# Kernel tuning notes

Hardware: AMD Instinct MI355X
Metric: run time of the kernel (lower is better)

Reference implementation:

```python
import jax, jax.numpy as jnp
import numpy as np

B, N, DIM = 32, 1024, 768
H, S, D = 16, 4, 64  # num_heads, num_subheads (L=H*S=64), attn_dim


def setup_inputs() -> dict:
    key = jax.random.key(0)
    k1, k2, k3, k4 = jax.random.split(key, 4)
    x = jax.random.normal(k1, (B, N, DIM), dtype=jnp.float32)
    eos_indices = jax.random.randint(k2, (B,), 0, N)
    # q_emb: original shape (1,H,S,1,D); singleton dims dropped -> (H,S,D)
    q_emb = jax.random.normal(k3, (H, S, D), dtype=jnp.float32)
    # k Linear(dim -> H*D), xavier-uniform weight, zero bias (share_kv: v == k)
    limit = float(np.sqrt(6.0 / (DIM + H * D)))
    Wk = jax.random.uniform(k4, (DIM, H * D), dtype=jnp.float32, minval=-limit, maxval=limit)
    bk = jnp.zeros((H * D,), dtype=jnp.float32)
    return {"x": x, "eos_indices": eos_indices, "q_emb": q_emb, "Wk": Wk, "bk": bk}


def reference(x, eos_indices, q_emb, Wk, bk):
    # x: (B,N,dim); shared k/v projection -> (B,N,H,D)
    kv = (x @ Wk + bk).reshape(x.shape[0], x.shape[1], H, D)
    scale = D ** -0.5
    # Avoid the torch expand over subheads: contract directly.
    # logits: (B,H,S,N)
    logits = jnp.einsum("hsd,bnhd->bhsn", q_emb * scale, kv)
    # eos masking: positions strictly after eos index are masked out
    mask = jnp.arange(x.shape[1])[None, None, None, :] > eos_indices[:, None, None, None]
    logits = jnp.where(mask, -jnp.inf, logits)
    attn = jax.nn.softmax(logits, axis=-1)
    # weighted sum over N -> (B,H,S,D) -> (B,L,D)
    out = jnp.einsum("bhsn,bnhd->bhsd", attn, kv)
    return out.reshape(x.shape[0], H * S, D)
```

## Files before the change

kernel.cpp:

```cpp
#include <hip/hip_runtime.h>
#include <hip/hip_bf16.h>
#include <stdint.h>

typedef float  f32x4  __attribute__((ext_vector_type(4)));
typedef __bf16 bf16x4 __attribute__((ext_vector_type(4)));
typedef __bf16 bf16x8 __attribute__((ext_vector_type(8)));
typedef unsigned int u32x2 __attribute__((ext_vector_type(2)));
typedef unsigned int u32x4 __attribute__((ext_vector_type(4)));

#define AS1 __attribute__((address_space(1)))
#define AS3 __attribute__((address_space(3)))

__device__ __forceinline__ void async_load16(const void* g, void* lds) {
    __builtin_amdgcn_global_load_lds((const AS1 unsigned int*)g,
                                     (AS3 unsigned int*)lds, 16, 0, 0);
}

__global__ __launch_bounds__(256) void qw_kernel(const float* __restrict__ q_emb,
                                                 const float* __restrict__ wk,
                                                 __bf16* __restrict__ qwT) {
    __shared__ float qlds[256];
    __shared__ float part[4096];
    const int t = threadIdx.x;
    const int kc = blockIdx.x;
    const int h  = blockIdx.y;
    const int k0 = kc * 64;
    qlds[t] = q_emb[h * 256 + t] * 0.125f;
    __syncthreads();
    const int dseg = t & 15;
    const int krow = t >> 4;
#pragma unroll
    for (int i = 0; i < 4; ++i) {
        const int k = i * 16 + krow;
        f32x4 wv = *(const f32x4*)&wk[(size_t)(k0 + k) * 1024 + h * 64 + dseg * 4];
#pragma unroll
        for (int s = 0; s < 4; ++s) {
            float p = qlds[s * 64 + dseg * 4 + 0] * wv[0]
                    + qlds[s * 64 + dseg * 4 + 1] * wv[1]
                    + qlds[s * 64 + dseg * 4 + 2] * wv[2]
                    + qlds[s * 64 + dseg * 4 + 3] * wv[3];
            part[k * 64 + s * 16 + dseg] = p;
        }
    }
    __syncthreads();
    const int k = t >> 2, s = t & 3;
    const float* pp = &part[k * 64 + s * 16];
    float sum = 0.f;
#pragma unroll
    for (int j = 0; j < 16; ++j) sum += pp[j];
    qwT[(h * 4 + s) * 768 + k0 + k] = (__bf16)sum;
}

__global__ __launch_bounds__(512) void logits_kernel(const float* __restrict__ x,
                                                     const __bf16* __restrict__ qwT,
                                                     const int* __restrict__ eos_idx,
                                                     float* __restrict__ Lg,
                                                     float* __restrict__ partials) {
    __shared__ char smem[49152];
    char* Bl = smem;
    char* Al = smem + 16384;
    const int t = threadIdx.x, l = t & 63, w = t >> 6;
    const int m0 = blockIdx.x * 128;
    const int bb = m0 >> 10, n0 = m0 & 1023;
    const int chunk = blockIdx.x & 7;
    const int wrA = (w >> 1) * 32;
    const int wcB = (w & 1) * 32;

    f32x4 acc[2][2];
#pragma unroll
    for (int i = 0; i < 2; ++i)
#pragma unroll
        for (int j = 0; j < 2; ++j) acc[i][j] = (f32x4)0.f;

    const int Bcol = t >> 3, Bseg = t & 7;
    const __bf16* qsrc = qwT + Bcol * 768 + (Bseg ^ (Bcol & 7)) * 8;
    const int Arow0 = t >> 4;
    const int Aseg = t & 15;

    f32x4 av[4];
    async_load16(qsrc, Bl + t * 16);
#pragma unroll
    for (int i = 0; i < 4; ++i)
        av[i] = *(const f32x4*)&x[(size_t)(m0 + i * 32 + Arow0) * 768 + Aseg * 4];
#pragma unroll
    for (int i = 0; i < 4; ++i) {
        const int row = i * 32 + Arow0;
        bf16x4 vv = {(__bf16)av[i][0], (__bf16)av[i][1], (__bf16)av[i][2], (__bf16)av[i][3]};
        *(bf16x4*)(Al + ((row * 128 + Aseg * 8) ^ ((row & 7) << 4))) = vv;
    }
    asm volatile("s_waitcnt vmcnt(0)" ::: "memory");
    __syncthreads();

    int buf = 0;
    for (int step = 0; step < 12; ++step) {
        const int nbuf = buf ^ 1;
        const bool more = (step + 1) < 12;
        if (more) {
            const int kt = (step + 1) * 64;
            async_load16(qsrc + kt, Bl + nbuf * 8192 + t * 16);
#pragma unroll
            for (int i = 0; i < 4; ++i)
                av[i] = *(const f32x4*)&x[(size_t)(m0 + i * 32 + Arow0) * 768 + kt + Aseg * 4];
        }
#pragma unroll
        for (int kh = 0; kh < 2; ++kh) {
            const int u = kh * 4 + (l >> 4);
            bf16x8 af[2], bfr[2];
#pragma unroll
            for (int i = 0; i < 2; ++i) {
                const int row = wrA + i * 16 + (l & 15);
                af[i] = *(const bf16x8*)(Al + buf * 16384 +
                                         ((row * 128 + u * 16) ^ ((row & 7) << 4)));
            }
#pragma unroll
            for (int j = 0; j < 2; ++j) {
                const int col = wcB + j * 16 + (l & 15);
                bfr[j] = *(const bf16x8*)(Bl + buf * 8192 +
                                          ((col * 128 + u * 16) ^ ((col & 7) << 4)));
            }
#pragma unroll
            for (int i = 0; i < 2; ++i)
#pragma unroll
                for (int j = 0; j < 2; ++j)
                    acc[i][j] = __builtin_amdgcn_mfma_f32_16x16x32_bf16(
                        af[i], bfr[j], acc[i][j], 0, 0, 0);
        }
        if (more) {
#pragma unroll
            for (int i = 0; i < 4; ++i) {
                const int row = i * 32 + Arow0;
                bf16x4 vv = {(__bf16)av[i][0], (__bf16)av[i][1], (__bf16)av[i][2], (__bf16)av[i][3]};
                *(bf16x4*)(Al + nbuf * 16384 + ((row * 128 + Aseg * 8) ^ ((row & 7) << 4))) = vv;
            }
        }
        asm volatile("s_waitcnt vmcnt(0)" ::: "memory");
        __syncthreads();
        buf = nbuf;
    }

#pragma unroll
    for (int i = 0; i < 2; ++i)
#pragma unroll
        for (int j = 0; j < 2; ++j) {
            const int hs = wcB + j * 16 + (l & 15);
            const int nb = wrA + i * 16 + (l >> 4) * 4;
            *(f32x4*)(smem + ((hs * 512 + nb * 4) ^ ((hs & 7) << 4))) = acc[i][j];
        }
    __syncthreads();
    const int eosb = eos_idx[bb];
    const int hs = t >> 3;
    f32x4 vv[4];
    float mx = -INFINITY;
#pragma unroll
    for (int i = 0; i < 4; ++i) {
        const int seg = (t & 7) + i * 8;
        f32x4 v = *(const f32x4*)(smem + ((hs * 512 + seg * 16) ^ ((hs & 7) << 4)));
#pragma unroll
        for (int j = 0; j < 4; ++j) {
            if (n0 + seg * 4 + j > eosb) v[j] = -INFINITY;
            mx = fmaxf(mx, v[j]);
        }
        vv[i] = v;
        *(f32x4*)&Lg[(size_t)bb * 65536 + hs * 1024 + n0 + seg * 4] = v;
    }
#pragma unroll
    for (int off = 1; off < 8; off <<= 1) mx = fmaxf(mx, __shfl_xor(mx, off));
    float sl = 0.f;
    if (mx > -INFINITY) {
#pragma unroll
        for (int i = 0; i < 4; ++i)
#pragma unroll
            for (int j = 0; j < 4; ++j) sl += __expf(vv[i][j] - mx);
    }
#pragma unroll
    for (int off = 1; off < 8; off <<= 1) sl += __shfl_xor(sl, off);
    if ((t & 7) == 0) {
        float2 st = {mx, sl};
        *(float2*)&partials[(size_t)(((bb * 8 + chunk) * 64) + hs) * 2] = st;
    }
}

__global__ __launch_bounds__(256) void pv_kernel(const float* __restrict__ x,
                                                 const float* __restrict__ Lg,
                                                 const float* __restrict__ partials,
                                                 float* __restrict__ y) {
    __shared__ char smem[32768];
    char* Pl = smem;
    char* Xl = smem + 16384;
    const int t = threadIdx.x, l = t & 63, w = t >> 6;
    const int vid = (blockIdx.x & 7) * 48 + (blockIdx.x >> 3);
    const int b = vid / 12, kc = vid % 12;
    const int k0 = kc * 64;
    const int wrA = (w >> 1) * 32, wcB = (w & 1) * 32;
    const float* Lgb = Lg + (size_t)b * 65536;
    const float* xb = x + (size_t)b * 786432 + k0 + l;
    const int fK = ((l & 7) << 4) | (((l >> 3) & 1) << 3);

    const int r0 = t >> 3, r1 = 32 + (t >> 3);
    float m0r, i0r, m1r, i1r;
    {
        const float* pb = partials + (size_t)b * 1024;
        float m = -INFINITY, m2 = -INFINITY;
#pragma unroll
        for (int c = 0; c < 8; ++c) {
            m  = fmaxf(m,  pb[(c * 64 + r0) * 2]);
            m2 = fmaxf(m2, pb[(c * 64 + r1) * 2]);
        }
        float s = 0.f, s2 = 0.f;
#pragma unroll
        for (int c = 0; c < 8; ++c) {
            float2 p0 = *(const float2*)&pb[(c * 64 + r0) * 2];
            float2 p1 = *(const float2*)&pb[(c * 64 + r1) * 2];
            s  += p0.y * __expf(p0.x - m);
            s2 += p1.y * __expf(p1.x - m2);
        }
        m0r = m; i0r = 1.0f / s;
        m1r = m2; i1r = 1.0f / s2;
    }
    const int n0s0 = (((t & 7) ^ (r0 & 7)) * 8);
    const int n0s1 = (((t & 7) ^ (r1 & 7)) * 8);

    f32x4 acc[2][2];
#pragma unroll
    for (int i = 0; i < 2; ++i)
#pragma unroll
        for (int j = 0; j < 2; ++j) acc[i][j] = (f32x4)0.f;

    float xv[16];
#pragma unroll
    for (int ii = 0; ii < 2; ++ii) {
        const int r = ii ? r1 : r0;
        const int ns = ii ? n0s1 : n0s0;
        const float mr = ii ? m1r : m0r, ir = ii ? i1r : i0r;
        f32x4 lo = *(const f32x4*)&Lgb[(size_t)r * 1024 + ns];
        f32x4 hi = *(const f32x4*)&Lgb[(size_t)r * 1024 + ns + 4];
        bf16x8 pk;
#pragma unroll
        for (int j = 0; j < 4; ++j) pk[j]     = (__bf16)(__expf(lo[j] - mr) * ir);
#pragma unroll
        for (int j = 0; j < 4; ++j) pk[4 + j] = (__bf16)(__expf(hi[j] - mr) * ir);
        *(bf16x8*)(Pl + ii * 4096 + t * 16) = pk;
    }
#pragma unroll
    for (int i = 0; i < 4; ++i)
#pragma unroll
        for (int j = 0; j < 4; ++j)
            xv[i * 4 + j] = xb[(size_t)(i * 16 + w * 4 + j) * 768];
#pragma unroll
    for (int i = 0; i < 4; ++i) {
        bf16x4 vv = {(__bf16)xv[i * 4 + 0], (__bf16)xv[i * 4 + 1],
                     (__bf16)xv[i * 4 + 2], (__bf16)xv[i * 4 + 3]};
        const int nb2 = (i * 16 + w * 4) * 2;
        *(bf16x4*)(Xl + ((l * 128 + nb2) ^ fK)) = vv;
    }
    __syncthreads();

    int buf = 0;
    for (int step = 0; step < 16; ++step) {
        const int nbuf = buf ^ 1;
        const bool more = (step + 1) < 16;
        if (more) {
            const int nt = (step + 1) * 64;
#pragma unroll
            for (int ii = 0; ii < 2; ++ii) {
                const int r = ii ? r1 : r0;
                const int ns = ii ? n0s1 : n0s0;
                const float mr = ii ? m1r : m0r, ir = ii ? i1r : i0r;
                f32x4 lo = *(const f32x4*)&Lgb[(size_t)r * 1024 + nt + ns];
                f32x4 hi = *(const f32x4*)&Lgb[(size_t)r * 1024 + nt + ns + 4];
                bf16x8 pk;
#pragma unroll
                for (int j = 0; j < 4; ++j) pk[j]     = (__bf16)(__expf(lo[j] - mr) * ir);
#pragma unroll
                for (int j = 0; j < 4; ++j) pk[4 + j] = (__bf16)(__expf(hi[j] - mr) * ir);
                *(bf16x8*)(Pl + nbuf * 8192 + ii * 4096 + t * 16) = pk;
            }
#pragma unroll
            for (int i = 0; i < 4; ++i)
#pragma unroll
                for (int j = 0; j < 4; ++j)
                    xv[i * 4 + j] = xb[(size_t)(nt + i * 16 + w * 4 + j) * 768];
        }
#pragma unroll
        for (int kh = 0; kh < 2; ++kh) {
            const int u = kh * 4 + (l >> 4);
            bf16x8 af[2], bfr[2];
#pragma unroll
            for (int i = 0; i < 2; ++i) {
                const int row = wrA + i * 16 + (l & 15);
                af[i] = *(const bf16x8*)(Pl + buf * 8192 +
                                         ((row * 128 + u * 16) ^ ((row & 7) << 4)));
            }
#pragma unroll
            for (int j = 0; j < 2; ++j) {
                const int kcol = wcB + j * 16 + (l & 15);
                const int fKc = ((kcol & 7) << 4) | (((kcol >> 3) & 1) << 3);
                const int addrA = kcol * 128 + kh * 64 + (l >> 4) * 16;
                u32x2 lo = *(const u32x2*)(Xl + buf * 8192 + (addrA ^ fKc));
                u32x2 hi = *(const u32x2*)(Xl + buf * 8192 + ((addrA + 8) ^ fKc));
                u32x4 uu = {lo[0], lo[1], hi[0], hi[1]};
                bfr[j] = __builtin_bit_cast(bf16x8, uu);
            }
#pragma unroll
            for (int i = 0; i < 2; ++i)
#pragma unroll
                for (int j = 0; j < 2; ++j)
                    acc[i][j] = __builtin_amdgcn_mfma_f32_16x16x32_bf16(
                        af[i], bfr[j], acc[i][j], 0, 0, 0);
        }
        if (more) {
#pragma unroll
            for (int i = 0; i < 4; ++i) {
                bf16x4 vv = {(__bf16)xv[i * 4 + 0], (__bf16)xv[i * 4 + 1],
                             (__bf16)xv[i * 4 + 2], (__bf16)xv[i * 4 + 3]};
                const int nb2 = (i * 16 + w * 4) * 2;
                *(bf16x4*)(Xl + nbuf * 8192 + ((l * 128 + nb2) ^ fK)) = vv;
            }
        }
        __syncthreads();
        buf = nbuf;
    }

#pragma unroll
    for (int i = 0; i < 2; ++i)
#pragma unroll
        for (int j = 0; j < 2; ++j) {
            const int kcol = wcB + j * 16 + (l & 15);
#pragma unroll
            for (int r = 0; r < 4; ++r) {
                const int hs2 = wrA + i * 16 + (l >> 4) * 4 + r;
                *(float*)(smem + ((hs2 * 256 + kcol * 4) ^ ((hs2 & 7) << 4))) = acc[i][j][r];
            }
        }
    __syncthreads();
    const int hs2 = t >> 2;
#pragma unroll
    for (int i = 0; i < 4; ++i) {
        const int seg = (t & 3) + i * 4;
        f32x4 v = *(const f32x4*)(smem + ((hs2 * 256 + seg * 16) ^ ((hs2 & 7) << 4)));
        *(f32x4*)&y[(size_t)(b * 64 + hs2) * 768 + k0 + seg * 4] = v;
    }
}

__global__ __launch_bounds__(256) void out_kernel(const float* __restrict__ y,
                                                  const float* __restrict__ wk,
                                                  const float* __restrict__ bk,
                                                  float* __restrict__ out) {
    __shared__ float ylds[8 * 768];
    __shared__ float red[2048];
    const int t = threadIdx.x;
    const int vid = (blockIdx.x & 7) * 32 + (blockIdx.x >> 3);
    const int h = vid >> 4, bp = vid & 15;
#pragma unroll
    for (int r = 0; r < 8; ++r) {
        const int gb = bp * 2 + (r >> 2);
        const int hs = h * 4 + (r & 3);
#pragma unroll
        for (int i = 0; i < 3; ++i)
            ylds[r * 768 + i * 256 + t] = y[(size_t)(gb * 64 + hs) * 768 + i * 256 + t];
    }
    __syncthreads();
    const int kp = t >> 6, d = t & 63;
    float acc[8] = {0.f, 0.f, 0.f, 0.f, 0.f, 0.f, 0.f, 0.f};
    for (int i = 0; i < 48; ++i) {
        const int k = kp * 192 + i * 4;
        const float wv0 = wk[(size_t)(k + 0) * 1024 + h * 64 + d];
        const float wv1 = wk[(size_t)(k + 1) * 1024 + h * 64 + d];
        const float wv2 = wk[(size_t)(k + 2) * 1024 + h * 64 + d];
        const float wv3 = wk[(size_t)(k + 3) * 1024 + h * 64 + d];
#pragma unroll
        for (int r = 0; r < 8; ++r) {
            f32x4 yv = *(const f32x4*)&ylds[r * 768 + k];
            acc[r] += yv[0] * wv0 + yv[1] * wv1 + yv[2] * wv2 + yv[3] * wv3;
        }
    }
#pragma unroll
    for (int r = 0; r < 8; ++r) red[(r * 64 + d) * 4 + kp] = acc[r];
    __syncthreads();
#pragma unroll
    for (int i = 0; i < 2; ++i) {
        const int o = i * 256 + t;
        const int r = o >> 6, dd = o & 63;
        f32x4 pv = *(const f32x4*)&red[o * 4];
        const float s = pv[0] + pv[1] + pv[2] + pv[3] + bk[h * 64 + dd];
        const int gb = bp * 2 + (r >> 2);
        out[(size_t)(gb * 64 + h * 4 + (r & 3)) * 64 + dd] = s;
    }
}

extern "C" void kernel_launch(void* const* d_in, const int* in_sizes, int n_in,
                              void* d_out, int out_size, void* d_ws, size_t ws_size,
                              hipStream_t stream) {
    const float* x     = (const float*)d_in[0];
    const int*   eos   = (const int*)d_in[1];
    const float* q_emb = (const float*)d_in[2];
    const float* Wk    = (const float*)d_in[3];
    const float* bk    = (const float*)d_in[4];
    float* out = (float*)d_out;

    char* ws = (char*)d_ws;
    __bf16* qwT      = (__bf16*)ws;
    float*  Lg       = (float*)(ws + 131072);
    float*  partials = (float*)(ws + 131072 + 8388608);
    float*  y        = (float*)(ws + 131072 + 8388608 + 131072);

    qw_kernel<<<dim3(12, 16), 256, 0, stream>>>(q_emb, Wk, qwT);
    logits_kernel<<<dim3(256), 512, 0, stream>>>(x, qwT, eos, Lg, partials);
    pv_kernel<<<dim3(384), 256, 0, stream>>>(x, Lg, partials, y);
    out_kernel<<<dim3(256), 256, 0, stream>>>(y, Wk, bk, out);
}
```

Baseline: 63.83 us.

## Halve tile sizes in logits and PV kernels to double grid parallelism

The logits kernel now processes 64 rows per block instead of 128, doubling the grid to 512 blocks and using 16 softmax partial chunks per batch. The PV kernel splits the sequence dimension into two halves, doubling its grid to 768 blocks and writing two partial y buffers, which the out kernel sums when loading. Launch bounds are tightened so more blocks fit per CU. The intent is to fill the 256 CUs better on this memory-bound pipeline, at the cost of extra partial-sum traffic, an extra y buffer read, and less reuse per block.

```diff
diff --git a/kernel.cpp b/kernel.cpp
--- a/kernel.cpp
+++ b/kernel.cpp
@@ -51,42 +51,41 @@
     qwT[(h * 4 + s) * 768 + k0 + k] = (__bf16)sum;
 }
 
-__global__ __launch_bounds__(512) void logits_kernel(const float* __restrict__ x,
-                                                     const __bf16* __restrict__ qwT,
-                                                     const int* __restrict__ eos_idx,
-                                                     float* __restrict__ Lg,
-                                                     float* __restrict__ partials) {
-    __shared__ char smem[49152];
+__global__ __launch_bounds__(512, 4) void logits_kernel(const float* __restrict__ x,
+                                                        const __bf16* __restrict__ qwT,
+                                                        const int* __restrict__ eos_idx,
+                                                        float* __restrict__ Lg,
+                                                        float* __restrict__ partials) {
+    __shared__ char smem[32768];
     char* Bl = smem;
     char* Al = smem + 16384;
     const int t = threadIdx.x, l = t & 63, w = t >> 6;
-    const int m0 = blockIdx.x * 128;
+    const int m0 = blockIdx.x * 64;
     const int bb = m0 >> 10, n0 = m0 & 1023;
-    const int chunk = blockIdx.x & 7;
-    const int wrA = (w >> 1) * 32;
-    const int wcB = (w & 1) * 32;
-
-    f32x4 acc[2][2];
-#pragma unroll
-    for (int i = 0; i < 2; ++i)
-#pragma unroll
-        for (int j = 0; j < 2; ++j) acc[i][j] = (f32x4)0.f;
+    const int chunk = (m0 >> 6) & 15;
+    const int wm = (w >> 1) * 16;
+    const int wh = (w & 1) * 32;
+
+    f32x4 acc[2];
+    acc[0] = (f32x4)0.f; acc[1] = (f32x4)0.f;
 
     const int Bcol = t >> 3, Bseg = t & 7;
     const __bf16* qsrc = qwT + Bcol * 768 + (Bseg ^ (Bcol & 7)) * 8;
-    const int Arow0 = t >> 4;
-    const int Aseg = t & 15;
-
-    f32x4 av[4];
+    const int Arow = t >> 3;
+    const float* xrow = &x[(size_t)(m0 + Arow) * 768 + (t & 7) * 8];
+    const int Adst = (Arow * 128 + (t & 7) * 16) ^ ((Arow & 7) << 4);
+
+    f32x4 av0, av1;
     async_load16(qsrc, Bl + t * 16);
-#pragma unroll
-    for (int i = 0; i < 4; ++i)
-        av[i] = *(const f32x4*)&x[(size_t)(m0 + i * 32 + Arow0) * 768 + Aseg * 4];
-#pragma unroll
-    for (int i = 0; i < 4; ++i) {
-        const int row = i * 32 + Arow0;
-        bf16x4 vv = {(__bf16)av[i][0], (__bf16)av[i][1], (__bf16)av[i][2], (__bf16)av[i][3]};
-        *(bf16x4*)(Al + ((row * 128 + Aseg * 8) ^ ((row & 7) << 4))) = vv;
+    av0 = *(const f32x4*)(xrow);
+    av1 = *(const f32x4*)(xrow + 4);
+    {
+        bf16x8 v;
+        v[0] = (__bf16)av0[0]; v[1] = (__bf16)av0[1];
+        v[2] = (__bf16)av0[2]; v[3] = (__bf16)av0[3];
+        v[4] = (__bf16)av1[0]; v[5] = (__bf16)av1[1];
+        v[6] = (__bf16)av1[2]; v[7] = (__bf16)av1[3];
+        *(bf16x8*)(Al + Adst) = v;
     }
     asm volatile("s_waitcnt vmcnt(0)" ::: "memory");
     __syncthreads();
@@ -98,40 +97,33 @@
         if (more) {
             const int kt = (step + 1) * 64;
             async_load16(qsrc + kt, Bl + nbuf * 8192 + t * 16);
-#pragma unroll
-            for (int i = 0; i < 4; ++i)
-                av[i] = *(const f32x4*)&x[(size_t)(m0 + i * 32 + Arow0) * 768 + kt + Aseg * 4];
+            av0 = *(const f32x4*)(xrow + kt);
+            av1 = *(const f32x4*)(xrow + kt + 4);
         }
 #pragma unroll
         for (int kh = 0; kh < 2; ++kh) {
             const int u = kh * 4 + (l >> 4);
-            bf16x8 af[2], bfr[2];
-#pragma unroll
-            for (int i = 0; i < 2; ++i) {
-                const int row = wrA + i * 16 + (l & 15);
-                af[i] = *(const bf16x8*)(Al + buf * 16384 +
-                                         ((row * 128 + u * 16) ^ ((row & 7) << 4)));
-            }
+            const int arow = wm + (l & 15);
+            bf16x8 af = *(const bf16x8*)(Al + buf * 8192 +
+                                         ((arow * 128 + u * 16) ^ ((arow & 7) << 4)));
+            bf16x8 bfr[2];
 #pragma unroll
             for (int j = 0; j < 2; ++j) {
-                const int col = wcB + j * 16 + (l & 15);
+                const int col = wh + j * 16 + (l & 15);
                 bfr[j] = *(const bf16x8*)(Bl + buf * 8192 +
                                           ((col * 128 + u * 16) ^ ((col & 7) << 4)));
             }
 #pragma unroll
-            for (int i = 0; i < 2; ++i)
-#pragma unroll
-                for (int j = 0; j < 2; ++j)
-                    acc[i][j] = __builtin_amdgcn_mfma_f32_16x16x32_bf16(
-                        af[i], bfr[j], acc[i][j], 0, 0, 0);
+            for (int j = 0; j < 2; ++j)
+                acc[j] = __builtin_amdgcn_mfma_f32_16x16x32_bf16(af, bfr[j], acc[j], 0, 0, 0);
         }
         if (more) {
-#pragma unroll
-            for (int i = 0; i < 4; ++i) {
-                const int row = i * 32 + Arow0;
-                bf16x4 vv = {(__bf16)av[i][0], (__bf16)av[i][1], (__bf16)av[i][2], (__bf16)av[i][3]};
-                *(bf16x4*)(Al + nbuf * 16384 + ((row * 128 + Aseg * 8) ^ ((row & 7) << 4))) = vv;
-            }
+            bf16x8 v;
+            v[0] = (__bf16)av0[0]; v[1] = (__bf16)av0[1];
+            v[2] = (__bf16)av0[2]; v[3] = (__bf16)av0[3];
+            v[4] = (__bf16)av1[0]; v[5] = (__bf16)av1[1];
+            v[6] = (__bf16)av1[2]; v[7] = (__bf16)av1[3];
+            *(bf16x8*)(Al + nbuf * 8192 + Adst) = v;
         }
         asm volatile("s_waitcnt vmcnt(0)" ::: "memory");
         __syncthreads();
@@ -139,58 +131,54 @@
     }
 
 #pragma unroll
-    for (int i = 0; i < 2; ++i)
-#pragma unroll
-        for (int j = 0; j < 2; ++j) {
-            const int hs = wcB + j * 16 + (l & 15);
-            const int nb = wrA + i * 16 + (l >> 4) * 4;
-            *(f32x4*)(smem + ((hs * 512 + nb * 4) ^ ((hs & 7) << 4))) = acc[i][j];
-        }
+    for (int j = 0; j < 2; ++j) {
+        const int hs = wh + j * 16 + (l & 15);
+        const int nb = wm + (l >> 4) * 4;
+        *(f32x4*)(smem + ((hs * 256 + nb * 4) ^ ((hs & 7) << 4))) = acc[j];
+    }
     __syncthreads();
     const int eosb = eos_idx[bb];
-    const int hs = t >> 3;
-    f32x4 vv[4];
+    const int hs = t >> 3, seg = t & 7;
+    const int fH = (hs & 7) << 4;
+    f32x4 v0 = *(const f32x4*)(smem + ((hs * 256 + seg * 32) ^ fH));
+    f32x4 v1 = *(const f32x4*)(smem + ((hs * 256 + seg * 32 + 16) ^ fH));
+    const int nbase = n0 + seg * 8;
     float mx = -INFINITY;
 #pragma unroll
-    for (int i = 0; i < 4; ++i) {
-        const int seg = (t & 7) + i * 8;
-        f32x4 v = *(const f32x4*)(smem + ((hs * 512 + seg * 16) ^ ((hs & 7) << 4)));
-#pragma unroll
-        for (int j = 0; j < 4; ++j) {
-            if (n0 + seg * 4 + j > eosb) v[j] = -INFINITY;
-            mx = fmaxf(mx, v[j]);
-        }
-        vv[i] = v;
-        *(f32x4*)&Lg[(size_t)bb * 65536 + hs * 1024 + n0 + seg * 4] = v;
-    }
+    for (int j = 0; j < 4; ++j) {
+        if (nbase + j > eosb) v0[j] = -INFINITY;
+        if (nbase + 4 + j > eosb) v1[j] = -INFINITY;
+        mx = fmaxf(mx, fmaxf(v0[j], v1[j]));
+    }
+    *(f32x4*)&Lg[(size_t)bb * 65536 + hs * 1024 + nbase] = v0;
+    *(f32x4*)&Lg[(size_t)bb * 65536 + hs * 1024 + nbase + 4] = v1;
 #pragma unroll
     for (int off = 1; off < 8; off <<= 1) mx = fmaxf(mx, __shfl_xor(mx, off));
     float sl = 0.f;
     if (mx > -INFINITY) {
 #pragma unroll
-        for (int i = 0; i < 4; ++i)
-#pragma unroll
-            for (int j = 0; j < 4; ++j) sl += __expf(vv[i][j] - mx);
+        for (int j = 0; j < 4; ++j) sl += __expf(v0[j] - mx) + __expf(v1[j] - mx);
     }
 #pragma unroll
     for (int off = 1; off < 8; off <<= 1) sl += __shfl_xor(sl, off);
-    if ((t & 7) == 0) {
+    if (seg == 0) {
         float2 st = {mx, sl};
-        *(float2*)&partials[(size_t)(((bb * 8 + chunk) * 64) + hs) * 2] = st;
-    }
-}
-
-__global__ __launch_bounds__(256) void pv_kernel(const float* __restrict__ x,
-                                                 const float* __restrict__ Lg,
-                                                 const float* __restrict__ partials,
-                                                 float* __restrict__ y) {
+        *(float2*)&partials[(size_t)(((bb * 16 + chunk) * 64) + hs) * 2] = st;
+    }
+}
+
+__global__ __launch_bounds__(256, 3) void pv_kernel(const float* __restrict__ x,
+                                                    const float* __restrict__ Lg,
+                                                    const float* __restrict__ partials,
+                                                    float* __restrict__ y) {
     __shared__ char smem[32768];
     char* Pl = smem;
     char* Xl = smem + 16384;
     const int t = threadIdx.x, l = t & 63, w = t >> 6;
-    const int vid = (blockIdx.x & 7) * 48 + (blockIdx.x >> 3);
-    const int b = vid / 12, kc = vid % 12;
-    const int k0 = kc * 64;
+    const int vid = (blockIdx.x & 7) * 96 + (blockIdx.x >> 3);
+    const int b = vid / 24, rem = vid % 24;
+    const int kc = rem % 12, nh = rem / 12;
+    const int k0 = kc * 64, nbase = nh * 512;
     const int wrA = (w >> 1) * 32, wcB = (w & 1) * 32;
     const float* Lgb = Lg + (size_t)b * 65536;
     const float* xb = x + (size_t)b * 786432 + k0 + l;
@@ -199,16 +187,16 @@
     const int r0 = t >> 3, r1 = 32 + (t >> 3);
     float m0r, i0r, m1r, i1r;
     {
-        const float* pb = partials + (size_t)b * 1024;
+        const float* pb = partials + (size_t)b * 2048;
         float m = -INFINITY, m2 = -INFINITY;
 #pragma unroll
-        for (int c = 0; c < 8; ++c) {
+        for (int c = 0; c < 16; ++c) {
             m  = fmaxf(m,  pb[(c * 64 + r0) * 2]);
             m2 = fmaxf(m2, pb[(c * 64 + r1) * 2]);
         }
         float s = 0.f, s2 = 0.f;
 #pragma unroll
-        for (int c = 0; c < 8; ++c) {
+        for (int c = 0; c < 16; ++c) {
             float2 p0 = *(const float2*)&pb[(c * 64 + r0) * 2];
             float2 p1 = *(const float2*)&pb[(c * 64 + r1) * 2];
             s  += p0.y * __expf(p0.x - m);
@@ -227,54 +215,48 @@
         for (int j = 0; j < 2; ++j) acc[i][j] = (f32x4)0.f;
 
     float xv[16];
-#pragma unroll
-    for (int ii = 0; ii < 2; ++ii) {
-        const int r = ii ? r1 : r0;
-        const int ns = ii ? n0s1 : n0s0;
-        const float mr = ii ? m1r : m0r, ir = ii ? i1r : i0r;
-        f32x4 lo = *(const f32x4*)&Lgb[(size_t)r * 1024 + ns];
-        f32x4 hi = *(const f32x4*)&Lgb[(size_t)r * 1024 + ns + 4];
+    f32x4 plo0, phi0, plo1, phi1;
+
+    plo0 = *(const f32x4*)&Lgb[(size_t)r0 * 1024 + nbase + n0s0];
+    phi0 = *(const f32x4*)&Lgb[(size_t)r0 * 1024 + nbase + n0s0 + 4];
+    plo1 = *(const f32x4*)&Lgb[(size_t)r1 * 1024 + nbase + n0s1];
+    phi1 = *(const f32x4*)&Lgb[(size_t)r1 * 1024 + nbase + n0s1 + 4];
+#pragma unroll
+    for (int i = 0; i < 4; ++i)
+#pragma unroll
+        for (int j = 0; j < 4; ++j)
+            xv[i * 4 + j] = xb[(size_t)(nbase + i * 16 + w * 4 + j) * 768];
+    {
         bf16x8 pk;
 #pragma unroll
-        for (int j = 0; j < 4; ++j) pk[j]     = (__bf16)(__expf(lo[j] - mr) * ir);
-#pragma unroll
-        for (int j = 0; j < 4; ++j) pk[4 + j] = (__bf16)(__expf(hi[j] - mr) * ir);
-        *(bf16x8*)(Pl + ii * 4096 + t * 16) = pk;
-    }
-#pragma unroll
-    for (int i = 0; i < 4; ++i)
-#pragma unroll
-        for (int j = 0; j < 4; ++j)
-            xv[i * 4 + j] = xb[(size_t)(i * 16 + w * 4 + j) * 768];
-#pragma unroll
-    for (int i = 0; i < 4; ++i) {
-        bf16x4 vv = {(__bf16)xv[i * 4 + 0], (__bf16)xv[i * 4 + 1],
-                     (__bf16)xv[i * 4 + 2], (__bf16)xv[i * 4 + 3]};
-        const int nb2 = (i * 16 + w * 4) * 2;
-        *(bf16x4*)(Xl + ((l * 128 + nb2) ^ fK)) = vv;
+        for (int j = 0; j < 4; ++j) pk[j]     = (__bf16)(__expf(plo0[j] - m0r) * i0r);
+#pragma unroll
+        for (int j = 0; j < 4; ++j) pk[4 + j] = (__bf16)(__expf(phi0[j] - m0r) * i0r);
+        *(bf16x8*)(Pl + t * 16) = pk;
+#pragma unroll
+        for (int j = 0; j < 4; ++j) pk[j]     = (__bf16)(__expf(plo1[j] - m1r) * i1r);
+#pragma unroll
+        for (int j = 0; j < 4; ++j) pk[4 + j] = (__bf16)(__expf(phi1[j] - m1r) * i1r);
+        *(bf16x8*)(Pl + 4096 + t * 16) = pk;
+#pragma unroll
+        for (int i = 0; i < 4; ++i) {
+            bf16x4 vv = {(__bf16)xv[i * 4 + 0], (__bf16)xv[i * 4 + 1],
+                         (__bf16)xv[i * 4 + 2], (__bf16)xv[i * 4 + 3]};
+            *(bf16x4*)(Xl + ((l * 128 + (i * 16 + w * 4) * 2) ^ fK)) = vv;
+        }
     }
     __syncthreads();
 
     int buf = 0;
-    for (int step = 0; step < 16; ++step) {
+    for (int step = 0; step < 8; ++step) {
         const int nbuf = buf ^ 1;
-        const bool more = (step + 1) < 16;
+        const bool more = (step + 1) < 8;
         if (more) {
-            const int nt = (step + 1) * 64;
-#pragma unroll
-            for (int ii = 0; ii < 2; ++ii) {
-                const int r = ii ? r1 : r0;
-                const int ns = ii ? n0s1 : n0s0;
-                const float mr = ii ? m1r : m0r, ir = ii ? i1r : i0r;
-                f32x4 lo = *(const f32x4*)&Lgb[(size_t)r * 1024 + nt + ns];
-                f32x4 hi = *(const f32x4*)&Lgb[(size_t)r * 1024 + nt + ns + 4];
-                bf16x8 pk;
-#pragma unroll
-                for (int j = 0; j < 4; ++j) pk[j]     = (__bf16)(__expf(lo[j] - mr) * ir);
-#pragma unroll
-                for (int j = 0; j < 4; ++j) pk[4 + j] = (__bf16)(__expf(hi[j] - mr) * ir);
-                *(bf16x8*)(Pl + nbuf * 8192 + ii * 4096 + t * 16) = pk;
-            }
+            const int nt = nbase + (step + 1) * 64;
+            plo0 = *(const f32x4*)&Lgb[(size_t)r0 * 1024 + nt + n0s0];
+            phi0 = *(const f32x4*)&Lgb[(size_t)r0 * 1024 + nt + n0s0 + 4];
+            plo1 = *(const f32x4*)&Lgb[(size_t)r1 * 1024 + nt + n0s1];
+            phi1 = *(const f32x4*)&Lgb[(size_t)r1 * 1024 + nt + n0s1 + 4];
 #pragma unroll
             for (int i = 0; i < 4; ++i)
 #pragma unroll
@@ -309,12 +291,22 @@
                         af[i], bfr[j], acc[i][j], 0, 0, 0);
         }
         if (more) {
+            bf16x8 pk;
+#pragma unroll
+            for (int j = 0; j < 4; ++j) pk[j]     = (__bf16)(__expf(plo0[j] - m0r) * i0r);
+#pragma unroll
+            for (int j = 0; j < 4; ++j) pk[4 + j] = (__bf16)(__expf(phi0[j] - m0r) * i0r);
+            *(bf16x8*)(Pl + nbuf * 8192 + t * 16) = pk;
+#pragma unroll
+            for (int j = 0; j < 4; ++j) pk[j]     = (__bf16)(__expf(plo1[j] - m1r) * i1r);
+#pragma unroll
+            for (int j = 0; j < 4; ++j) pk[4 + j] = (__bf16)(__expf(phi1[j] - m1r) * i1r);
+            *(bf16x8*)(Pl + nbuf * 8192 + 4096 + t * 16) = pk;
 #pragma unroll
             for (int i = 0; i < 4; ++i) {
                 bf16x4 vv = {(__bf16)xv[i * 4 + 0], (__bf16)xv[i * 4 + 1],
                              (__bf16)xv[i * 4 + 2], (__bf16)xv[i * 4 + 3]};
-                const int nb2 = (i * 16 + w * 4) * 2;
-                *(bf16x4*)(Xl + nbuf * 8192 + ((l * 128 + nb2) ^ fK)) = vv;
+                *(bf16x4*)(Xl + nbuf * 8192 + ((l * 128 + (i * 16 + w * 4) * 2) ^ fK)) = vv;
             }
         }
         __syncthreads();
@@ -333,12 +325,13 @@
             }
         }
     __syncthreads();
+    float* yh = y + (size_t)nh * 1572864;
     const int hs2 = t >> 2;
 #pragma unroll
     for (int i = 0; i < 4; ++i) {
         const int seg = (t & 3) + i * 4;
         f32x4 v = *(const f32x4*)(smem + ((hs2 * 256 + seg * 16) ^ ((hs2 & 7) << 4)));
-        *(f32x4*)&y[(size_t)(b * 64 + hs2) * 768 + k0 + seg * 4] = v;
+        *(f32x4*)&yh[(size_t)(b * 64 + hs2) * 768 + k0 + seg * 4] = v;
     }
 }
 
@@ -356,8 +349,10 @@
         const int gb = bp * 2 + (r >> 2);
         const int hs = h * 4 + (r & 3);
 #pragma unroll
-        for (int i = 0; i < 3; ++i)
-            ylds[r * 768 + i * 256 + t] = y[(size_t)(gb * 64 + hs) * 768 + i * 256 + t];
+        for (int i = 0; i < 3; ++i) {
+            const size_t idx = (size_t)(gb * 64 + hs) * 768 + i * 256 + t;
+            ylds[r * 768 + i * 256 + t] = y[idx] + y[idx + 1572864];
+        }
     }
     __syncthreads();
     const int kp = t >> 6, d = t & 63;
@@ -401,11 +396,11 @@
     char* ws = (char*)d_ws;
     __bf16* qwT      = (__bf16*)ws;
     float*  Lg       = (float*)(ws + 131072);
-    float*  partials = (float*)(ws + 131072 + 8388608);
-    float*  y        = (float*)(ws + 131072 + 8388608 + 131072);
+    float*  partials = (float*)(ws + 8519680);
+    float*  y        = (float*)(ws + 8781824);
 
     qw_kernel<<<dim3(12, 16), 256, 0, stream>>>(q_emb, Wk, qwT);
-    logits_kernel<<<dim3(256), 512, 0, stream>>>(x, qwT, eos, Lg, partials);
-    pv_kernel<<<dim3(384), 256, 0, stream>>>(x, Lg, partials, y);
+    logits_kernel<<<dim3(512), 512, 0, stream>>>(x, qwT, eos, Lg, partials);
+    pv_kernel<<<dim3(768), 256, 0, stream>>>(x, Lg, partials, y);
     out_kernel<<<dim3(256), 256, 0, stream>>>(y, Wk, bk, out);
 }
```

New measurement: 65.10 us. About the same (+2.0%).

## Store logits in bf16 and fuse output projection into pv kernel with atomics

Applied to the files above, without the earlier changes.

Logits are now written to workspace as bf16 instead of fp32, which halves that intermediate's traffic. The softmax partial statistics are taken from the rounded values so they stay consistent. The separate out_kernel is removed: each pv block multiplies its 64-column slice of y by the matching Wk rows and atomically adds into the output, which a new bias_init kernel fills with the bias first. The pv staging loop is also reorganised into STAGE/COMPUTE lambdas with a min-occupancy hint. The cost is extra atomics, nondeterministic summation order and bf16 rounding of the logits.

```diff
diff --git a/kernel.cpp b/kernel.cpp
--- a/kernel.cpp
+++ b/kernel.cpp
@@ -14,6 +14,12 @@
 __device__ __forceinline__ void async_load16(const void* g, void* lds) {
     __builtin_amdgcn_global_load_lds((const AS1 unsigned int*)g,
                                      (AS3 unsigned int*)lds, 16, 0, 0);
+}
+
+__global__ __launch_bounds__(256) void bias_init(const float* __restrict__ bk,
+                                                 float* __restrict__ out) {
+    const int idx = blockIdx.x * 256 + threadIdx.x;
+    out[idx] = bk[((idx >> 8) & 15) * 64 + (idx & 63)];
 }
 
 __global__ __launch_bounds__(256) void qw_kernel(const float* __restrict__ q_emb,
@@ -54,7 +60,7 @@
 __global__ __launch_bounds__(512) void logits_kernel(const float* __restrict__ x,
                                                      const __bf16* __restrict__ qwT,
                                                      const int* __restrict__ eos_idx,
-                                                     float* __restrict__ Lg,
+                                                     __bf16* __restrict__ Lg,
                                                      float* __restrict__ partials) {
     __shared__ char smem[49152];
     char* Bl = smem;
@@ -148,20 +154,23 @@
         }
     __syncthreads();
     const int eosb = eos_idx[bb];
-    const int hs = t >> 3;
-    f32x4 vv[4];
+    const int hs = t >> 3, seg7 = t & 7;
+    const int fH = (hs & 7) << 4;
     float mx = -INFINITY;
+    bf16x4 pk4[4];
 #pragma unroll
     for (int i = 0; i < 4; ++i) {
-        const int seg = (t & 7) + i * 8;
-        f32x4 v = *(const f32x4*)(smem + ((hs * 512 + seg * 16) ^ ((hs & 7) << 4)));
+        const int seg = seg7 + i * 8;
+        f32x4 v = *(const f32x4*)(smem + ((hs * 512 + seg * 16) ^ fH));
+        bf16x4 pk;
 #pragma unroll
         for (int j = 0; j < 4; ++j) {
-            if (n0 + seg * 4 + j > eosb) v[j] = -INFINITY;
-            mx = fmaxf(mx, v[j]);
-        }
-        vv[i] = v;
-        *(f32x4*)&Lg[(size_t)bb * 65536 + hs * 1024 + n0 + seg * 4] = v;
+            const float f = (n0 + seg * 4 + j > eosb) ? -INFINITY : v[j];
+            pk[j] = (__bf16)f;
+            mx = fmaxf(mx, (float)pk[j]);
+        }
+        pk4[i] = pk;
+        *(bf16x4*)&Lg[(size_t)bb * 65536 + hs * 1024 + n0 + seg * 4] = pk;
     }
 #pragma unroll
     for (int off = 1; off < 8; off <<= 1) mx = fmaxf(mx, __shfl_xor(mx, off));
@@ -170,20 +179,21 @@
 #pragma unroll
         for (int i = 0; i < 4; ++i)
 #pragma unroll
-            for (int j = 0; j < 4; ++j) sl += __expf(vv[i][j] - mx);
+            for (int j = 0; j < 4; ++j) sl += __expf((float)pk4[i][j] - mx);
     }
 #pragma unroll
     for (int off = 1; off < 8; off <<= 1) sl += __shfl_xor(sl, off);
-    if ((t & 7) == 0) {
+    if (seg7 == 0) {
         float2 st = {mx, sl};
         *(float2*)&partials[(size_t)(((bb * 8 + chunk) * 64) + hs) * 2] = st;
     }
 }
 
-__global__ __launch_bounds__(256) void pv_kernel(const float* __restrict__ x,
-                                                 const float* __restrict__ Lg,
-                                                 const float* __restrict__ partials,
-                                                 float* __restrict__ y) {
+__global__ __launch_bounds__(256, 3) void pv_kernel(const float* __restrict__ x,
+                                                    const __bf16* __restrict__ Lg,
+                                                    const float* __restrict__ partials,
+                                                    const float* __restrict__ wk,
+                                                    float* __restrict__ out_p) {
     __shared__ char smem[32768];
     char* Pl = smem;
     char* Xl = smem + 16384;
@@ -192,7 +202,7 @@
     const int b = vid / 12, kc = vid % 12;
     const int k0 = kc * 64;
     const int wrA = (w >> 1) * 32, wcB = (w & 1) * 32;
-    const float* Lgb = Lg + (size_t)b * 65536;
+    const __bf16* Lgb = Lg + (size_t)b * 65536;
     const float* xb = x + (size_t)b * 786432 + k0 + l;
     const int fK = ((l & 7) << 4) | (((l >> 3) & 1) << 3);
 
@@ -226,61 +236,32 @@
 #pragma unroll
         for (int j = 0; j < 2; ++j) acc[i][j] = (f32x4)0.f;
 
-    float xv[16];
-#pragma unroll
-    for (int ii = 0; ii < 2; ++ii) {
-        const int r = ii ? r1 : r0;
-        const int ns = ii ? n0s1 : n0s0;
-        const float mr = ii ? m1r : m0r, ir = ii ? i1r : i0r;
-        f32x4 lo = *(const f32x4*)&Lgb[(size_t)r * 1024 + ns];
-        f32x4 hi = *(const f32x4*)&Lgb[(size_t)r * 1024 + ns + 4];
+    auto STAGE = [&](int bufb, int T) {
+        bf16x8 g0 = *(const bf16x8*)&Lgb[(size_t)r0 * 1024 + T * 64 + n0s0];
+        bf16x8 g1 = *(const bf16x8*)&Lgb[(size_t)r1 * 1024 + T * 64 + n0s1];
+        float xv[16];
+#pragma unroll
+        for (int i_ = 0; i_ < 4; ++i_)
+#pragma unroll
+            for (int j_ = 0; j_ < 4; ++j_)
+                xv[i_ * 4 + j_] = xb[(size_t)(T * 64 + i_ * 16 + w * 4 + j_) * 768];
         bf16x8 pk;
 #pragma unroll
-        for (int j = 0; j < 4; ++j) pk[j]     = (__bf16)(__expf(lo[j] - mr) * ir);
-#pragma unroll
-        for (int j = 0; j < 4; ++j) pk[4 + j] = (__bf16)(__expf(hi[j] - mr) * ir);
-        *(bf16x8*)(Pl + ii * 4096 + t * 16) = pk;
-    }
-#pragma unroll
-    for (int i = 0; i < 4; ++i)
-#pragma unroll
-        for (int j = 0; j < 4; ++j)
-            xv[i * 4 + j] = xb[(size_t)(i * 16 + w * 4 + j) * 768];
-#pragma unroll
-    for (int i = 0; i < 4; ++i) {
-        bf16x4 vv = {(__bf16)xv[i * 4 + 0], (__bf16)xv[i * 4 + 1],
-                     (__bf16)xv[i * 4 + 2], (__bf16)xv[i * 4 + 3]};
-        const int nb2 = (i * 16 + w * 4) * 2;
-        *(bf16x4*)(Xl + ((l * 128 + nb2) ^ fK)) = vv;
-    }
-    __syncthreads();
-
-    int buf = 0;
-    for (int step = 0; step < 16; ++step) {
-        const int nbuf = buf ^ 1;
-        const bool more = (step + 1) < 16;
-        if (more) {
-            const int nt = (step + 1) * 64;
-#pragma unroll
-            for (int ii = 0; ii < 2; ++ii) {
-                const int r = ii ? r1 : r0;
-                const int ns = ii ? n0s1 : n0s0;
-                const float mr = ii ? m1r : m0r, ir = ii ? i1r : i0r;
-                f32x4 lo = *(const f32x4*)&Lgb[(size_t)r * 1024 + nt + ns];
-                f32x4 hi = *(const f32x4*)&Lgb[(size_t)r * 1024 + nt + ns + 4];
-                bf16x8 pk;
-#pragma unroll
-                for (int j = 0; j < 4; ++j) pk[j]     = (__bf16)(__expf(lo[j] - mr) * ir);
-#pragma unroll
-                for (int j = 0; j < 4; ++j) pk[4 + j] = (__bf16)(__expf(hi[j] - mr) * ir);
-                *(bf16x8*)(Pl + nbuf * 8192 + ii * 4096 + t * 16) = pk;
-            }
-#pragma unroll
-            for (int i = 0; i < 4; ++i)
-#pragma unroll
-                for (int j = 0; j < 4; ++j)
-                    xv[i * 4 + j] = xb[(size_t)(nt + i * 16 + w * 4 + j) * 768];
-        }
+        for (int j_ = 0; j_ < 8; ++j_)
+            pk[j_] = (__bf16)(__expf((float)g0[j_] - m0r) * i0r);
+        *(bf16x8*)(Pl + bufb * 8192 + t * 16) = pk;
+#pragma unroll
+        for (int j_ = 0; j_ < 8; ++j_)
+            pk[j_] = (__bf16)(__expf((float)g1[j_] - m1r) * i1r);
+        *(bf16x8*)(Pl + bufb * 8192 + 4096 + t * 16) = pk;
+#pragma unroll
+        for (int i_ = 0; i_ < 4; ++i_) {
+            bf16x4 vv = {(__bf16)xv[i_ * 4 + 0], (__bf16)xv[i_ * 4 + 1],
+                         (__bf16)xv[i_ * 4 + 2], (__bf16)xv[i_ * 4 + 3]};
+            *(bf16x4*)(Xl + bufb * 8192 + ((l * 128 + (i_ * 16 + w * 4) * 2) ^ fK)) = vv;
+        }
+    };
+    auto COMPUTE = [&](int bufb) {
 #pragma unroll
         for (int kh = 0; kh < 2; ++kh) {
             const int u = kh * 4 + (l >> 4);
@@ -288,7 +269,7 @@
 #pragma unroll
             for (int i = 0; i < 2; ++i) {
                 const int row = wrA + i * 16 + (l & 15);
-                af[i] = *(const bf16x8*)(Pl + buf * 8192 +
+                af[i] = *(const bf16x8*)(Pl + bufb * 8192 +
                                          ((row * 128 + u * 16) ^ ((row & 7) << 4)));
             }
 #pragma unroll
@@ -296,8 +277,8 @@
                 const int kcol = wcB + j * 16 + (l & 15);
                 const int fKc = ((kcol & 7) << 4) | (((kcol >> 3) & 1) << 3);
                 const int addrA = kcol * 128 + kh * 64 + (l >> 4) * 16;
-                u32x2 lo = *(const u32x2*)(Xl + buf * 8192 + (addrA ^ fKc));
-                u32x2 hi = *(const u32x2*)(Xl + buf * 8192 + ((addrA + 8) ^ fKc));
+                u32x2 lo = *(const u32x2*)(Xl + bufb * 8192 + (addrA ^ fKc));
+                u32x2 hi = *(const u32x2*)(Xl + bufb * 8192 + ((addrA + 8) ^ fKc));
                 u32x4 uu = {lo[0], lo[1], hi[0], hi[1]};
                 bfr[j] = __builtin_bit_cast(bf16x8, uu);
             }
@@ -308,17 +289,16 @@
                     acc[i][j] = __builtin_amdgcn_mfma_f32_16x16x32_bf16(
                         af[i], bfr[j], acc[i][j], 0, 0, 0);
         }
-        if (more) {
-#pragma unroll
-            for (int i = 0; i < 4; ++i) {
-                bf16x4 vv = {(__bf16)xv[i * 4 + 0], (__bf16)xv[i * 4 + 1],
-                             (__bf16)xv[i * 4 + 2], (__bf16)xv[i * 4 + 3]};
-                const int nb2 = (i * 16 + w * 4) * 2;
-                *(bf16x4*)(Xl + nbuf * 8192 + ((l * 128 + nb2) ^ fK)) = vv;
-            }
-        }
+    };
+
+    STAGE(0, 0);
+    __syncthreads();
+    int buf = 0;
+    for (int step = 0; step < 16; ++step) {
+        if (step + 1 < 16) STAGE(buf ^ 1, step + 1);
+        COMPUTE(buf);
         __syncthreads();
-        buf = nbuf;
+        buf ^= 1;
     }
 
 #pragma unroll
@@ -333,58 +313,34 @@
             }
         }
     __syncthreads();
-    const int hs2 = t >> 2;
-#pragma unroll
-    for (int i = 0; i < 4; ++i) {
-        const int seg = (t & 3) + i * 4;
-        f32x4 v = *(const f32x4*)(smem + ((hs2 * 256 + seg * 16) ^ ((hs2 & 7) << 4)));
-        *(f32x4*)&y[(size_t)(b * 64 + hs2) * 768 + k0 + seg * 4] = v;
-    }
-}
-
-__global__ __launch_bounds__(256) void out_kernel(const float* __restrict__ y,
-                                                  const float* __restrict__ wk,
-                                                  const float* __restrict__ bk,
-                                                  float* __restrict__ out) {
-    __shared__ float ylds[8 * 768];
-    __shared__ float red[2048];
-    const int t = threadIdx.x;
-    const int vid = (blockIdx.x & 7) * 32 + (blockIdx.x >> 3);
-    const int h = vid >> 4, bp = vid & 15;
-#pragma unroll
-    for (int r = 0; r < 8; ++r) {
-        const int gb = bp * 2 + (r >> 2);
-        const int hs = h * 4 + (r & 3);
-#pragma unroll
-        for (int i = 0; i < 3; ++i)
-            ylds[r * 768 + i * 256 + t] = y[(size_t)(gb * 64 + hs) * 768 + i * 256 + t];
-    }
-    __syncthreads();
-    const int kp = t >> 6, d = t & 63;
-    float acc[8] = {0.f, 0.f, 0.f, 0.f, 0.f, 0.f, 0.f, 0.f};
-    for (int i = 0; i < 48; ++i) {
-        const int k = kp * 192 + i * 4;
-        const float wv0 = wk[(size_t)(k + 0) * 1024 + h * 64 + d];
-        const float wv1 = wk[(size_t)(k + 1) * 1024 + h * 64 + d];
-        const float wv2 = wk[(size_t)(k + 2) * 1024 + h * 64 + d];
-        const float wv3 = wk[(size_t)(k + 3) * 1024 + h * 64 + d];
-#pragma unroll
-        for (int r = 0; r < 8; ++r) {
-            f32x4 yv = *(const f32x4*)&ylds[r * 768 + k];
-            acc[r] += yv[0] * wv0 + yv[1] * wv1 + yv[2] * wv2 + yv[3] * wv3;
-        }
-    }
-#pragma unroll
-    for (int r = 0; r < 8; ++r) red[(r * 64 + d) * 4 + kp] = acc[r];
-    __syncthreads();
-#pragma unroll
-    for (int i = 0; i < 2; ++i) {
-        const int o = i * 256 + t;
-        const int r = o >> 6, dd = o & 63;
-        f32x4 pv = *(const f32x4*)&red[o * 4];
-        const float s = pv[0] + pv[1] + pv[2] + pv[3] + bk[h * 64 + dd];
-        const int gb = bp * 2 + (r >> 2);
-        out[(size_t)(gb * 64 + h * 4 + (r & 3)) * 64 + dd] = s;
+
+    const int d = l;
+#pragma unroll
+    for (int hh = 0; hh < 4; ++hh) {
+        const int h = w * 4 + hh;
+        const float* wcol = &wk[(size_t)k0 * 1024 + h * 64 + d];
+        float ao0 = 0.f, ao1 = 0.f, ao2 = 0.f, ao3 = 0.f;
+#pragma unroll 4
+        for (int kq = 0; kq < 16; ++kq) {
+            const float wv0 = wcol[(size_t)(kq * 4 + 0) * 1024];
+            const float wv1 = wcol[(size_t)(kq * 4 + 1) * 1024];
+            const float wv2 = wcol[(size_t)(kq * 4 + 2) * 1024];
+            const float wv3 = wcol[(size_t)(kq * 4 + 3) * 1024];
+            const int hsb = h * 4;
+            f32x4 y0 = *(const f32x4*)(smem + (((hsb + 0) * 256 + kq * 16) ^ (((hsb + 0) & 7) << 4)));
+            f32x4 y1 = *(const f32x4*)(smem + (((hsb + 1) * 256 + kq * 16) ^ (((hsb + 1) & 7) << 4)));
+            f32x4 y2 = *(const f32x4*)(smem + (((hsb + 2) * 256 + kq * 16) ^ (((hsb + 2) & 7) << 4)));
+            f32x4 y3 = *(const f32x4*)(smem + (((hsb + 3) * 256 + kq * 16) ^ (((hsb + 3) & 7) << 4)));
+            ao0 += y0[0] * wv0 + y0[1] * wv1 + y0[2] * wv2 + y0[3] * wv3;
+            ao1 += y1[0] * wv0 + y1[1] * wv1 + y1[2] * wv2 + y1[3] * wv3;
+            ao2 += y2[0] * wv0 + y2[1] * wv1 + y2[2] * wv2 + y2[3] * wv3;
+            ao3 += y3[0] * wv0 + y3[1] * wv1 + y3[2] * wv2 + y3[3] * wv3;
+        }
+        float* ob = &out_p[(size_t)(b * 64 + h * 4) * 64 + d];
+        atomicAdd(ob +   0, ao0);
+        atomicAdd(ob +  64, ao1);
+        atomicAdd(ob + 128, ao2);
+        atomicAdd(ob + 192, ao3);
     }
 }
 
@@ -400,12 +356,11 @@
 
     char* ws = (char*)d_ws;
     __bf16* qwT      = (__bf16*)ws;
-    float*  Lg       = (float*)(ws + 131072);
-    float*  partials = (float*)(ws + 131072 + 8388608);
-    float*  y        = (float*)(ws + 131072 + 8388608 + 131072);
-
+    __bf16* Lg       = (__bf16*)(ws + 131072);
+    float*  partials = (float*)(ws + 131072 + 4194304);
+
+    bias_init<<<dim3(512), 256, 0, stream>>>(bk, out);
     qw_kernel<<<dim3(12, 16), 256, 0, stream>>>(q_emb, Wk, qwT);
     logits_kernel<<<dim3(256), 512, 0, stream>>>(x, qwT, eos, Lg, partials);
-    pv_kernel<<<dim3(384), 256, 0, stream>>>(x, Lg, partials, y);
-    out_kernel<<<dim3(256), 256, 0, stream>>>(y, Wk, bk, out);
-}
+    pv_kernel<<<dim3(384), 256, 0, stream>>>(x, Lg, partials, Wk, out);
+}
```

After: 66.30 us. +3.9%, slower.
